# Performance work log

Measured on AMD Instinct MI355X. Metric: run time of the kernel, lower is better.

Reference implementation:

```python
import jax, jax.numpy as jnp
import numpy as np

N = 100000
E = 1600000
IN_DIM = 128
HID = 64
TDIM = 16
OUT_DIM = 2
NEG_SLOPE = 0.01  # F.leaky_relu default


def _linear_params(key, fan_in, fan_out):
    kw, kb = jax.random.split(key)
    s = 1.0 / np.sqrt(fan_in)
    w = jax.random.uniform(kw, (fan_in, fan_out), jnp.float32, -s, s)
    b = jax.random.uniform(kb, (fan_out,), jnp.float32, -s, s)
    return w, b


def setup_inputs() -> dict:
    key = jax.random.key(0)
    ks = jax.random.split(key, 12)
    x = jax.random.normal(ks[0], (N, IN_DIM), jnp.float32)
    edge_index = jax.random.randint(ks[1], (2, E), 0, N, jnp.int32)
    edge_time = jax.random.uniform(ks[2], (E, 1), jnp.float32)

    lin1_w, lin1_b = _linear_params(ks[3], IN_DIM, HID)
    attn1_w, attn1_b = _linear_params(ks[4], 2 * HID + TDIM, 1)
    t1_w, t1_b = _linear_params(ks[5], 1, TDIM)

    lin2_w, lin2_b = _linear_params(ks[6], HID, HID)
    attn2_w, attn2_b = _linear_params(ks[7], 2 * HID + TDIM, 1)
    t2_w, t2_b = _linear_params(ks[8], 1, TDIM)

    cls_w, cls_b = _linear_params(ks[9], HID, OUT_DIM)

    return dict(x=x, edge_index=edge_index, edge_time=edge_time,
                lin1_w=lin1_w, lin1_b=lin1_b, attn1_w=attn1_w, attn1_b=attn1_b,
                t1_w=t1_w, t1_b=t1_b,
                lin2_w=lin2_w, lin2_b=lin2_b, attn2_w=attn2_w, attn2_b=attn2_b,
                t2_w=t2_w, t2_b=t2_b, cls_w=cls_w, cls_b=cls_b)


def _segment_softmax(a, index, num_segments):
    # PyG softmax over variable-size neighborhoods grouped by destination node
    m = jax.ops.segment_max(a, index, num_segments=num_segments)
    e = jnp.exp(a - m[index])
    s = jax.ops.segment_sum(e, index, num_segments=num_segments)
    return e / (s[index] + 1e-16)


def _temporal_gat_conv(x, src, dst, edge_time,
                       lin_w, lin_b, attn_w, attn_b, t_w, t_b):
    # TemporalEncoding: sin(Linear(1, time_dim)(t))  -> [E, TDIM]
    t_enc = jnp.sin(edge_time @ t_w + t_b)
    # lin applied per-edge to x_i and x_j == lin applied once at node level then gathered
    h = x @ lin_w + lin_b                      # [N, HID]
    h_i = h[dst]                               # [E, HID] target features
    h_j = h[src]                               # [E, HID] source features
    alpha_in = jnp.concatenate([h_i, h_j, t_enc], axis=1)   # [E, 2*HID+TDIM]
    alpha = jax.nn.leaky_relu(alpha_in @ attn_w + attn_b, NEG_SLOPE)  # [E, 1]
    alpha = _segment_softmax(alpha, dst, x.shape[0])
    msg = h_j * alpha                          # [E, HID]
    return jax.ops.segment_sum(msg, dst, num_segments=x.shape[0])  # aggr='add'


def reference(x, edge_index, edge_time,
              lin1_w, lin1_b, attn1_w, attn1_b, t1_w, t1_b,
              lin2_w, lin2_b, attn2_w, attn2_b, t2_w, t2_b,
              cls_w, cls_b):
    src = edge_index[0]  # j (source)
    dst = edge_index[1]  # i (target / softmax segment index)
    h = _temporal_gat_conv(x, src, dst, edge_time,
                           lin1_w, lin1_b, attn1_w, attn1_b, t1_w, t1_b)
    h = jax.nn.relu(h)
    # dropout p=0.3 is identity in eval mode
    h = _temporal_gat_conv(h, src, dst, edge_time,
                           lin2_w, lin2_b, attn2_w, attn2_b, t2_w, t2_b)
    return h @ cls_w + cls_b  # [N, OUT_DIM]
```

## Files before the change

kernel.cpp:

```cpp
#include <hip/hip_runtime.h>

typedef unsigned short u16;
typedef unsigned int u32;

typedef __attribute__((ext_vector_type(8))) short short8v;
typedef __attribute__((ext_vector_type(4))) float float4v;

__device__ __forceinline__ float bf2f(u16 u) {
    return __uint_as_float(((u32)u) << 16);
}
__device__ __forceinline__ u16 f2bf(float f) {
    u32 u = __float_as_uint(f);
    u32 r = (u + 0x7fffu + ((u >> 16) & 1u)) >> 16;
    return (u16)r;
}
__device__ __forceinline__ float ldf(const void* p, int i, int isf32) {
    return isf32 ? ((const float*)p)[i] : bf2f(((const u16*)p)[i]);
}

#define P_W1   0
#define P_W2   8192
#define P_B1   12288
#define P_B2   12352
#define P_A1W  12416
#define P_A1B  12560
#define P_T1W  12561
#define P_T1B  12577
#define P_A2W  12593
#define P_A2B  12737
#define P_T2W  12738
#define P_T2B  12754
#define P_CLSW 12770
#define P_CLSB 12898
#define P_TOT  12900

#define CH   4096
#define NCHB 256
#define CAP  128

#define W1F_ELEMS 16384
#define W2F_ELEMS 8192

__global__ __launch_bounds__(256) void detect_dtype(
    const u32* __restrict__ xw, int nwords, int* __restrict__ flag)
{
    __shared__ int sbad;
    if (threadIdx.x == 0) sbad = 0;
    __syncthreads();
    int bad = 0;
    for (int i = threadIdx.x; i < nwords; i += 256) {
        u32 w = xw[i];
        int ea = (w >> 7) & 0xff;
        if (ea >= 0xF0) bad = 1;
    }
    if (bad) sbad = 1;
    __syncthreads();
    if (threadIdx.x == 0) flag[0] = sbad;
}

__global__ __launch_bounds__(256) void prep_params(
    const void* l1w, const void* l1b, const void* a1w, const void* a1b,
    const void* t1w, const void* t1b, const void* l2w, const void* l2b,
    const void* a2w, const void* a2b, const void* t2w, const void* t2b,
    const void* clsw, const void* clsb,
    const int* __restrict__ flag, float* __restrict__ P)
{
    const int f = flag[0];
    const int t = blockIdx.x * 256 + threadIdx.x;
    const int stride = gridDim.x * 256;
#define SEG(src, off, cnt) for (int i = t; i < (cnt); i += stride) P[(off) + i] = ldf(src, i, f)
    SEG(l1w, P_W1, 8192);
    SEG(l2w, P_W2, 4096);
    SEG(l1b, P_B1, 64);
    SEG(l2b, P_B2, 64);
    SEG(a1w, P_A1W, 144);
    SEG(a1b, P_A1B, 1);
    SEG(t1w, P_T1W, 16);
    SEG(t1b, P_T1B, 16);
    SEG(a2w, P_A2W, 144);
    SEG(a2b, P_A2B, 1);
    SEG(t2w, P_T2W, 16);
    SEG(t2b, P_T2B, 16);
    SEG(clsw, P_CLSW, 128);
    SEG(clsb, P_CLSB, 2);
#undef SEG
}

__global__ __launch_bounds__(256) void prep_wfrags(
    const float* __restrict__ P,
    u16* __restrict__ w1h, u16* __restrict__ w1l,
    u16* __restrict__ w2h, u16* __restrict__ w2l)
{
    int e = blockIdx.x * 256 + threadIdx.x;
    if (e >= W1F_ELEMS + W2F_ELEMS) return;
    int idx, woff;
    u16 *dh, *dl;
    if (e < W1F_ELEMS) { idx = e; woff = P_W1; dh = w1h; dl = w1l; }
    else { idx = e - W1F_ELEMS; woff = P_W2; dh = w2h; dl = w2l; }
    int j = idx & 7;
    int l = (idx >> 3) & 63;
    int ctks = idx >> 9;
    int ct = ctks & 3;
    int ks = ctks >> 2;
    int k = ks * 32 + (l >> 4) * 8 + j;
    int col = ct * 16 + (l & 15);
    float wv = P[woff + k * 64 + col];
    u16 hh = f2bf(wv);
    dh[idx] = hh;
    dl[idx] = f2bf(wv - bf2f(hh));
}

template<int K, int XMODE>
__global__ __launch_bounds__(256) void node_gemm_mfma(
    const void* __restrict__ xin, const float* __restrict__ P,
    int BOFF, int AOFF, const int* __restrict__ flag,
    const u16* __restrict__ wfh, const u16* __restrict__ wfl,
    u32* __restrict__ houtb, float* __restrict__ si, float* __restrict__ sj,
    int nnodes)
{
    const int l = threadIdx.x & 63;
    const int w = threadIdx.x >> 6;
    const int cl = l & 15;
    const int cg = l >> 4;
    const int rowbase = blockIdx.x * 64 + w * 16;
    const bool xf32 = (XMODE == 0) ? (flag[0] != 0) : false;

    const int arow = rowbase + cl;
    const int arc = (arow < nnodes) ? arow : 0;
    const int kb = cg * 8;

    const u16* xb = (const u16*)xin;
    const float* xf = (const float*)xin;
    const short8v* bhp = (const short8v*)wfh;
    const short8v* blp = (const short8v*)wfl;

    float4v acc[4];
    #pragma unroll
    for (int ct = 0; ct < 4; ++ct) acc[ct] = (float4v){0.f, 0.f, 0.f, 0.f};

    #pragma unroll
    for (int ks = 0; ks < K / 32; ++ks) {
        short8v ah, al_;
        bool hasl = false;
        if (XMODE == 2 || !xf32) {
            ah = *(const short8v*)&xb[(size_t)arc * K + ks * 32 + kb];
            al_ = (short8v){0, 0, 0, 0, 0, 0, 0, 0};
        } else {
            float4 v0 = *(const float4*)&xf[(size_t)arc * K + ks * 32 + kb];
            float4 v1 = *(const float4*)&xf[(size_t)arc * K + ks * 32 + kb + 4];
            float fv[8] = { v0.x, v0.y, v0.z, v0.w, v1.x, v1.y, v1.z, v1.w };
            #pragma unroll
            for (int j = 0; j < 8; ++j) {
                u16 hh = f2bf(fv[j]);
                ah[j] = (short)hh;
                al_[j] = (short)f2bf(fv[j] - bf2f(hh));
            }
            hasl = true;
        }
        #pragma unroll
        for (int ct = 0; ct < 4; ++ct) {
            short8v bh = bhp[(ks * 4 + ct) * 64 + l];
            short8v bl = blp[(ks * 4 + ct) * 64 + l];
            acc[ct] = __builtin_amdgcn_mfma_f32_16x16x32_bf16(ah, bh, acc[ct], 0, 0, 0);
            acc[ct] = __builtin_amdgcn_mfma_f32_16x16x32_bf16(ah, bl, acc[ct], 0, 0, 0);
            if (hasl)
                acc[ct] = __builtin_amdgcn_mfma_f32_16x16x32_bf16(al_, bh, acc[ct], 0, 0, 0);
        }
    }

    #pragma unroll
    for (int r = 0; r < 4; ++r) {
        int node = rowbase + cg * 4 + r;
        float aiv = 0.f, ajv = 0.f;
        u16 hs[4];
        #pragma unroll
        for (int ct = 0; ct < 4; ++ct) {
            float v = acc[ct][r] + P[BOFF + ct * 16 + cl];
            aiv = fmaf(v, P[AOFF + ct * 16 + cl], aiv);
            ajv = fmaf(v, P[AOFF + 64 + ct * 16 + cl], ajv);
            hs[ct] = f2bf(v);
        }
        #pragma unroll
        for (int o = 1; o < 16; o <<= 1) {
            aiv += __shfl_xor(aiv, o);
            ajv += __shfl_xor(ajv, o);
        }
        if (node < nnodes) {
            u16* hp = (u16*)houtb + (size_t)node * 64 + cl;
            hp[0] = hs[0]; hp[16] = hs[1]; hp[32] = hs[2]; hp[48] = hs[3];
            if (cl == 0) { si[node] = aiv; sj[node] = ajv; }
        }
    }
}

__global__ __launch_bounds__(256) void count_chunks(
    const int* __restrict__ eid, int* __restrict__ chunkhist, int E)
{
    __shared__ int hist[NCHB];
    const int t = threadIdx.x, c = blockIdx.x;
    hist[t] = 0;
    __syncthreads();
    const int base = c * CH;
    #pragma unroll
    for (int i = 0; i < CH / 256; ++i) {
        int e = base + t + i * 256;
        if (e < E) atomicAdd(&hist[eid[e] >> 9], 1);
    }
    __syncthreads();
    chunkhist[c * NCHB + t] = hist[t];
}

__global__ __launch_bounds__(256) void scan_chunks(
    int* __restrict__ chunkhist, int* __restrict__ buckettot, int nchunks)
{
    __shared__ int s[512];
    const int b = blockIdx.x, t = threadIdx.x;
    int v0 = (t < nchunks) ? chunkhist[(size_t)t * NCHB + b] : 0;
    int v1 = (t + 256 < nchunks) ? chunkhist[(size_t)(t + 256) * NCHB + b] : 0;
    s[t] = v0; s[t + 256] = v1;
    __syncthreads();
    for (int off = 1; off < 512; off <<= 1) {
        int x0 = (t >= off) ? s[t - off] : 0;
        int x1 = s[t + 256 - off];
        __syncthreads();
        s[t] += x0; s[t + 256] += x1;
        __syncthreads();
    }
    if (t < nchunks) chunkhist[(size_t)t * NCHB + b] = s[t] - v0;
    if (t + 256 < nchunks) chunkhist[(size_t)(t + 256) * NCHB + b] = s[t + 256] - v1;
    if (t == 255) buckettot[b] = s[511];
}

__global__ __launch_bounds__(256) void bucket_start_scan(
    const int* __restrict__ buckettot, int* __restrict__ bucketstart,
    int* __restrict__ offs, int N)
{
    __shared__ int s[NCHB];
    const int b = threadIdx.x;
    int v = buckettot[b];
    s[b] = v;
    __syncthreads();
    for (int off = 1; off < NCHB; off <<= 1) {
        int x = (b >= off) ? s[b - off] : 0;
        __syncthreads();
        s[b] += x;
        __syncthreads();
    }
    bucketstart[b] = s[b] - v;
    if (b == NCHB - 1) { bucketstart[NCHB] = s[b]; offs[N] = s[b]; }
}

__global__ __launch_bounds__(256) void place_chunks(
    const int* __restrict__ ei, const void* __restrict__ et,
    const int* __restrict__ flag, const int* __restrict__ chunkhist,
    const int* __restrict__ bucketstart, int2* __restrict__ staging, int E)
{
    __shared__ int2 sorted[CH];
    __shared__ unsigned char bno[CH];
    __shared__ int hist[NCHB], lstart[NCHB], cur[NCHB], gb[NCHB];
    const int t = threadIdx.x, c = blockIdx.x;
    const int base = c * CH;
    const int f = flag[0];
    hist[t] = 0;
    gb[t] = bucketstart[t] + chunkhist[c * NCHB + t];
    __syncthreads();
    #pragma unroll
    for (int i = 0; i < CH / 256; ++i) {
        int e = base + t + i * 256;
        if (e < E) atomicAdd(&hist[ei[E + e] >> 9], 1);
    }
    __syncthreads();
    int v = hist[t];
    lstart[t] = v;
    __syncthreads();
    for (int off = 1; off < NCHB; off <<= 1) {
        int x = (t >= off) ? lstart[t - off] : 0;
        __syncthreads();
        lstart[t] += x;
        __syncthreads();
    }
    int ex = lstart[t] - v;
    __syncthreads();
    lstart[t] = ex;
    cur[t] = ex;
    __syncthreads();
    #pragma unroll
    for (int i = 0; i < CH / 256; ++i) {
        int e = base + t + i * 256;
        if (e < E) {
            int s_ = ei[e], d = ei[E + e];
            float tt = ldf(et, e, f);
            int b = d >> 9;
            int p = atomicAdd(&cur[b], 1);
            sorted[p] = make_int2(s_ | ((d & 511) << 17), __float_as_int(tt));
            bno[p] = (unsigned char)b;
        }
    }
    __syncthreads();
    const int cnt_tot = min(CH, E - base);
    for (int idx = t; idx < cnt_tot; idx += 256) {
        int b = bno[idx];
        staging[gb[b] + (idx - lstart[b])] = sorted[idx];
    }
}

__global__ __launch_bounds__(256) void bin_edges(
    const int2* __restrict__ staging, const int* __restrict__ bucketstart,
    int* __restrict__ offs, int2* __restrict__ csrA, int N)
{
    __shared__ int cnt[512], loc[512];
    const int b = blockIdx.x, t = threadIdx.x;
    const int beg = bucketstart[b], end = bucketstart[b + 1];
    const int nstart = b << 9;
    cnt[t] = 0; cnt[t + 256] = 0;
    __syncthreads();
    for (int i = beg + t; i < end; i += 256)
        atomicAdd(&cnt[(((u32)staging[i].x) >> 17) & 511], 1);
    __syncthreads();
    int v0 = cnt[t], v1 = cnt[t + 256];
    loc[t] = v0; loc[t + 256] = v1;
    __syncthreads();
    for (int off = 1; off < 512; off <<= 1) {
        int x0 = (t >= off) ? loc[t - off] : 0;
        int x1 = loc[t + 256 - off];
        __syncthreads();
        loc[t] += x0; loc[t + 256] += x1;
        __syncthreads();
    }
    int cur0 = beg + loc[t] - v0;
    int cur1 = beg + loc[t + 256] - v1;
    if (nstart + t < N) offs[nstart + t] = cur0;
    if (nstart + t + 256 < N) offs[nstart + t + 256] = cur1;
    cnt[t] = cur0; cnt[t + 256] = cur1;
    __syncthreads();
    for (int i = beg + t; i < end; i += 256) {
        int2 e = staging[i];
        int slot = atomicAdd(&cnt[(((u32)e.x) >> 17) & 511], 1);
        csrA[slot] = make_int2(e.x & 0x1ffff, e.y);
    }
}

__global__ __launch_bounds__(256) void temporal_pass(
    int2* __restrict__ csrA, int2* __restrict__ csrB,
    const float* __restrict__ P, int E)
{
    int i = blockIdx.x * 256 + threadIdx.x;
    if (i >= E) return;
    int2 e = csrA[i];
    float tt = __int_as_float(e.y);
    float td1 = P[P_A1B], td2 = P[P_A2B];
    #pragma unroll
    for (int k = 0; k < 16; ++k) {
        td1 += __sinf(fmaf(tt, P[P_T1W + k], P[P_T1B + k])) * P[P_A1W + 128 + k];
        td2 += __sinf(fmaf(tt, P[P_T2W + k], P[P_T2B + k])) * P[P_A2W + 128 + k];
    }
    csrA[i] = make_int2(e.x, __float_as_int(td1));
    csrB[i] = make_int2(e.x, __float_as_int(td2));
}

template<int MODE>
__global__ __launch_bounds__(256) void aggregate(
    const int* __restrict__ offs, const int2* __restrict__ csr2,
    const u32* __restrict__ hb,
    const float* __restrict__ si, const float* __restrict__ sjv,
    const float* __restrict__ P,
    u32* __restrict__ houtb, void* __restrict__ outp,
    const int* __restrict__ flag, int n)
{
    __shared__ int2 cache[4][2][CAP];
    const int wave = threadIdx.x >> 6;
    const int lane = threadIdx.x & 63;
    const int half = lane >> 5;
    const int hl = lane & 31;
    const int node = blockIdx.x * 8 + wave * 2 + half;
    const bool active = node < n;
    int beg = 0, end = 0;
    if (active) { beg = offs[node]; end = offs[node + 1]; }
    const int deg = end - beg;
    int2* cw = cache[wave][half];
    const float sii = active ? si[node] : 0.f;

    float ssum = 0.f;
    for (int idx = hl; idx < deg; idx += 32) {
        int2 st = csr2[beg + idx];
        float a = sii + sjv[st.x] + __int_as_float(st.y);
        a = (a > 0.f) ? a : 0.01f * a;
        float e = __expf(fminf(a, 80.f));
        if (idx < CAP) cw[idx] = make_int2(st.x, __float_as_int(e));
        ssum += e;
    }
    #pragma unroll
    for (int o = 16; o > 0; o >>= 1) ssum += __shfl_xor(ssum, o);

    const int degc = min(deg, CAP);
    const int degpad = (degc + 3) & ~3;
    if (hl < degpad - degc) cw[degc + hl] = make_int2(0, 0);

    float ax = 0.f, ay = 0.f;
    for (int j0 = 0; j0 < degpad; j0 += 4) {
        int2 s0 = cw[j0 + 0];
        int2 s1 = cw[j0 + 1];
        int2 s2 = cw[j0 + 2];
        int2 s3 = cw[j0 + 3];
        u32 p0 = hb[s0.x * 32 + hl];
        u32 p1 = hb[s1.x * 32 + hl];
        u32 p2 = hb[s2.x * 32 + hl];
        u32 p3 = hb[s3.x * 32 + hl];
        float e0 = __int_as_float(s0.y);
        float e1 = __int_as_float(s1.y);
        float e2 = __int_as_float(s2.y);
        float e3 = __int_as_float(s3.y);
        ax = fmaf(e0, __uint_as_float(p0 << 16), ax);
        ay = fmaf(e0, __uint_as_float(p0 & 0xffff0000u), ay);
        ax = fmaf(e1, __uint_as_float(p1 << 16), ax);
        ay = fmaf(e1, __uint_as_float(p1 & 0xffff0000u), ay);
        ax = fmaf(e2, __uint_as_float(p2 << 16), ax);
        ay = fmaf(e2, __uint_as_float(p2 & 0xffff0000u), ay);
        ax = fmaf(e3, __uint_as_float(p3 << 16), ax);
        ay = fmaf(e3, __uint_as_float(p3 & 0xffff0000u), ay);
    }
    for (int j = CAP; j < deg; ++j) {
        int2 st = csr2[beg + j];
        float a = sii + sjv[st.x] + __int_as_float(st.y);
        a = (a > 0.f) ? a : 0.01f * a;
        float e = __expf(fminf(a, 80.f));
        u32 pk = hb[st.x * 32 + hl];
        ax = fmaf(e, __uint_as_float(pk << 16), ax);
        ay = fmaf(e, __uint_as_float(pk & 0xffff0000u), ay);
    }

    if (!active) return;
    float inv = 1.0f / (ssum + 1e-16f);

    if (MODE == 0) {
        float r0 = fmaxf(ax * inv, 0.f);
        float r1 = fmaxf(ay * inv, 0.f);
        houtb[node * 32 + hl] = (u32)f2bf(r0) | ((u32)f2bf(r1) << 16);
    } else {
        float r0 = ax * inv, r1 = ay * inv;
        float l0 = r0 * P[P_CLSW + 4 * hl]     + r1 * P[P_CLSW + 4 * hl + 2];
        float l1 = r0 * P[P_CLSW + 4 * hl + 1] + r1 * P[P_CLSW + 4 * hl + 3];
        #pragma unroll
        for (int o = 16; o > 0; o >>= 1) {
            l0 += __shfl_xor(l0, o);
            l1 += __shfl_xor(l1, o);
        }
        if (hl == 0) {
            l0 += P[P_CLSB];
            l1 += P[P_CLSB + 1];
            if (flag[0]) {
                ((float2*)outp)[node] = make_float2(l0, l1);
            } else {
                ((u32*)outp)[node] = (u32)f2bf(l0) | ((u32)f2bf(l1) << 16);
            }
        }
    }
}

extern "C" void kernel_launch(void* const* d_in, const int* in_sizes, int n_in,
                              void* d_out, int out_size, void* d_ws, size_t ws_size,
                              hipStream_t stream)
{
    const void* x    = d_in[0];
    const int*  ei   = (const int*)d_in[1];
    const void* et   = d_in[2];
    const void* l1w  = d_in[3];
    const void* l1b  = d_in[4];
    const void* a1w  = d_in[5];
    const void* a1b  = d_in[6];
    const void* t1w  = d_in[7];
    const void* t1b  = d_in[8];
    const void* l2w  = d_in[9];
    const void* l2b  = d_in[10];
    const void* a2w  = d_in[11];
    const void* a2b  = d_in[12];
    const void* t2w  = d_in[13];
    const void* t2b  = d_in[14];
    const void* clsw = d_in[15];
    const void* clsb = d_in[16];

    const int N = in_sizes[0] / 128;
    const int E = in_sizes[2];
    const int nchunks = (E + CH - 1) / CH;
    const int nbkt = (N + 511) >> 9;

    char* ws = (char*)d_ws;
    size_t off = 0;
    auto A = [&](size_t bytes) -> char* {
        char* p = ws + off;
        off = (off + bytes + 255) & ~(size_t)255;
        return p;
    };
    int*   flag        = (int*)A(256);
    float* P           = (float*)A(P_TOT * 4);
    u16*   w1fh        = (u16*)A(W1F_ELEMS * 2);
    u16*   w1fl        = (u16*)A(W1F_ELEMS * 2);
    u16*   w2fh        = (u16*)A(W2F_ELEMS * 2);
    u16*   w2fl        = (u16*)A(W2F_ELEMS * 2);
    u32*   h1b         = (u32*)A((size_t)N * 32 * 4);
    float* si1         = (float*)A((size_t)N * 4);
    float* sj1         = (float*)A((size_t)N * 4);
    float* si2         = (float*)A((size_t)N * 4);
    float* sj2         = (float*)A((size_t)N * 4);
    int*   chunkhist   = (int*)A((size_t)nchunks * NCHB * 4);
    int*   buckettot   = (int*)A(NCHB * 4);
    int*   bucketstart = (int*)A((size_t)(NCHB + 1) * 4);
    int*   offs        = (int*)A((size_t)(N + 1) * 4);
    int2*  csrA        = (int2*)A((size_t)E * 8);
    int2*  csrB        = (int2*)A((size_t)E * 8);
    char*  unionr      = A((size_t)E * 8 < (size_t)N * 32 * 4
                           ? (size_t)N * 32 * 4 : (size_t)E * 8);
    int2*  staging     = (int2*)unionr;
    u32*   hagb        = (u32*)unionr;
    (void)ws_size; (void)n_in; (void)out_size;

    detect_dtype<<<1, 256, 0, stream>>>((const u32*)x, 4096, flag);

    prep_params<<<32, 256, 0, stream>>>(l1w, l1b, a1w, a1b, t1w, t1b,
                                        l2w, l2b, a2w, a2b, t2w, t2b,
                                        clsw, clsb, flag, P);

    prep_wfrags<<<(W1F_ELEMS + W2F_ELEMS) / 256, 256, 0, stream>>>(
        P, w1fh, w1fl, w2fh, w2fl);

    node_gemm_mfma<128, 0><<<(N + 63) / 64, 256, 0, stream>>>(
        x, P, P_B1, P_A1W, flag, w1fh, w1fl, h1b, si1, sj1, N);

    count_chunks<<<nchunks, 256, 0, stream>>>(ei + E, chunkhist, E);

    scan_chunks<<<NCHB, 256, 0, stream>>>(chunkhist, buckettot, nchunks);

    bucket_start_scan<<<1, 256, 0, stream>>>(buckettot, bucketstart, offs, N);

    place_chunks<<<nchunks, 256, 0, stream>>>(ei, et, flag, chunkhist,
                                              bucketstart, staging, E);

    bin_edges<<<nbkt, 256, 0, stream>>>(staging, bucketstart, offs, csrA, N);

    temporal_pass<<<(E + 255) / 256, 256, 0, stream>>>(csrA, csrB, P, E);

    aggregate<0><<<(N + 7) / 8, 256, 0, stream>>>(
        offs, csrA, h1b, si1, sj1, P, hagb, nullptr, flag, N);

    node_gemm_mfma<64, 2><<<(N + 63) / 64, 256, 0, stream>>>(
        hagb, P, P_B2, P_A2W, flag, w2fh, w2fl, h1b, si2, sj2, N);

    aggregate<1><<<(N + 7) / 8, 256, 0, stream>>>(
        offs, csrB, h1b, si2, sj2, P, nullptr, d_out, flag, N);
}
```

Baseline: 299.7 us.

## Fuse temporal encoding into aggregation and merge weight-fragment prep into param prep

Removes the separate temporal_pass kernel, which read csrA and wrote both csrA and csrB over all edges. Each aggregate kernel now computes the 16-term sine time encoding inline from the raw edge time, and both layers share a single CSR buffer. prep_wfrags is folded into prep_params, so one launch is gone. The gather loop is also unrolled from 4 to 8 outstanding loads, and the fp32 high-part split now truncates instead of rounding. The inline sine work adds compute to the aggregation kernels, and the truncated high part changes which bits go into the low correction term.

```diff
diff --git a/kernel.cpp b/kernel.cpp
--- a/kernel.cpp
+++ b/kernel.cpp
@@ -63,7 +63,9 @@
     const void* t1w, const void* t1b, const void* l2w, const void* l2b,
     const void* a2w, const void* a2b, const void* t2w, const void* t2b,
     const void* clsw, const void* clsb,
-    const int* __restrict__ flag, float* __restrict__ P)
+    const int* __restrict__ flag, float* __restrict__ P,
+    u16* __restrict__ w1h, u16* __restrict__ w1l,
+    u16* __restrict__ w2h, u16* __restrict__ w2l)
 {
     const int f = flag[0];
     const int t = blockIdx.x * 256 + threadIdx.x;
@@ -84,30 +86,24 @@
     SEG(clsw, P_CLSW, 128);
     SEG(clsb, P_CLSB, 2);
 #undef SEG
-}
-
-__global__ __launch_bounds__(256) void prep_wfrags(
-    const float* __restrict__ P,
-    u16* __restrict__ w1h, u16* __restrict__ w1l,
-    u16* __restrict__ w2h, u16* __restrict__ w2l)
-{
-    int e = blockIdx.x * 256 + threadIdx.x;
-    if (e >= W1F_ELEMS + W2F_ELEMS) return;
-    int idx, woff;
-    u16 *dh, *dl;
-    if (e < W1F_ELEMS) { idx = e; woff = P_W1; dh = w1h; dl = w1l; }
-    else { idx = e - W1F_ELEMS; woff = P_W2; dh = w2h; dl = w2l; }
-    int j = idx & 7;
-    int l = (idx >> 3) & 63;
-    int ctks = idx >> 9;
-    int ct = ctks & 3;
-    int ks = ctks >> 2;
-    int k = ks * 32 + (l >> 4) * 8 + j;
-    int col = ct * 16 + (l & 15);
-    float wv = P[woff + k * 64 + col];
-    u16 hh = f2bf(wv);
-    dh[idx] = hh;
-    dl[idx] = f2bf(wv - bf2f(hh));
+    for (int e = t; e < W1F_ELEMS + W2F_ELEMS; e += stride) {
+        int idx;
+        const void* wsrc;
+        u16 *dh, *dl;
+        if (e < W1F_ELEMS) { idx = e; wsrc = l1w; dh = w1h; dl = w1l; }
+        else { idx = e - W1F_ELEMS; wsrc = l2w; dh = w2h; dl = w2l; }
+        int j = idx & 7;
+        int l = (idx >> 3) & 63;
+        int ctks = idx >> 9;
+        int ct = ctks & 3;
+        int ks = ctks >> 2;
+        int k = ks * 32 + (l >> 4) * 8 + j;
+        int col = ct * 16 + (l & 15);
+        float wv = ldf(wsrc, k * 64 + col, f);
+        u16 hh = f2bf(wv);
+        dh[idx] = hh;
+        dl[idx] = f2bf(wv - bf2f(hh));
+    }
 }
 
 template<int K, int XMODE>
@@ -151,9 +147,10 @@
             float fv[8] = { v0.x, v0.y, v0.z, v0.w, v1.x, v1.y, v1.z, v1.w };
             #pragma unroll
             for (int j = 0; j < 8; ++j) {
-                u16 hh = f2bf(fv[j]);
-                ah[j] = (short)hh;
-                al_[j] = (short)f2bf(fv[j] - bf2f(hh));
+                u32 u = __float_as_uint(fv[j]);
+                ah[j] = (short)(u >> 16);
+                float hif = __uint_as_float(u & 0xffff0000u);
+                al_[j] = (short)f2bf(fv[j] - hif);
             }
             hasl = true;
         }
@@ -340,24 +337,6 @@
     }
 }
 
-__global__ __launch_bounds__(256) void temporal_pass(
-    int2* __restrict__ csrA, int2* __restrict__ csrB,
-    const float* __restrict__ P, int E)
-{
-    int i = blockIdx.x * 256 + threadIdx.x;
-    if (i >= E) return;
-    int2 e = csrA[i];
-    float tt = __int_as_float(e.y);
-    float td1 = P[P_A1B], td2 = P[P_A2B];
-    #pragma unroll
-    for (int k = 0; k < 16; ++k) {
-        td1 += __sinf(fmaf(tt, P[P_T1W + k], P[P_T1B + k])) * P[P_A1W + 128 + k];
-        td2 += __sinf(fmaf(tt, P[P_T2W + k], P[P_T2B + k])) * P[P_A2W + 128 + k];
-    }
-    csrA[i] = make_int2(e.x, __float_as_int(td1));
-    csrB[i] = make_int2(e.x, __float_as_int(td2));
-}
-
 template<int MODE>
 __global__ __launch_bounds__(256) void aggregate(
     const int* __restrict__ offs, const int2* __restrict__ csr2,
@@ -367,6 +346,11 @@
     u32* __restrict__ houtb, void* __restrict__ outp,
     const int* __restrict__ flag, int n)
 {
+    constexpr int TW = (MODE == 0) ? P_T1W : P_T2W;
+    constexpr int TB = (MODE == 0) ? P_T1B : P_T2B;
+    constexpr int AW = (MODE == 0) ? P_A1W : P_A2W;
+    constexpr int AB = (MODE == 0) ? P_A1B : P_A2B;
+
     __shared__ int2 cache[4][2][CAP];
     const int wave = threadIdx.x >> 6;
     const int lane = threadIdx.x & 63;
@@ -383,7 +367,12 @@
     float ssum = 0.f;
     for (int idx = hl; idx < deg; idx += 32) {
         int2 st = csr2[beg + idx];
-        float a = sii + sjv[st.x] + __int_as_float(st.y);
+        float tt = __int_as_float(st.y);
+        float td = P[AB];
+        #pragma unroll
+        for (int k = 0; k < 16; ++k)
+            td += __sinf(fmaf(tt, P[TW + k], P[TB + k])) * P[AW + 128 + k];
+        float a = sii + sjv[st.x] + td;
         a = (a > 0.f) ? a : 0.01f * a;
         float e = __expf(fminf(a, 80.f));
         if (idx < CAP) cw[idx] = make_int2(st.x, __float_as_int(e));
@@ -393,35 +382,32 @@
     for (int o = 16; o > 0; o >>= 1) ssum += __shfl_xor(ssum, o);
 
     const int degc = min(deg, CAP);
-    const int degpad = (degc + 3) & ~3;
+    const int degpad = (degc + 7) & ~7;
     if (hl < degpad - degc) cw[degc + hl] = make_int2(0, 0);
 
     float ax = 0.f, ay = 0.f;
-    for (int j0 = 0; j0 < degpad; j0 += 4) {
-        int2 s0 = cw[j0 + 0];
-        int2 s1 = cw[j0 + 1];
-        int2 s2 = cw[j0 + 2];
-        int2 s3 = cw[j0 + 3];
-        u32 p0 = hb[s0.x * 32 + hl];
-        u32 p1 = hb[s1.x * 32 + hl];
-        u32 p2 = hb[s2.x * 32 + hl];
-        u32 p3 = hb[s3.x * 32 + hl];
-        float e0 = __int_as_float(s0.y);
-        float e1 = __int_as_float(s1.y);
-        float e2 = __int_as_float(s2.y);
-        float e3 = __int_as_float(s3.y);
-        ax = fmaf(e0, __uint_as_float(p0 << 16), ax);
-        ay = fmaf(e0, __uint_as_float(p0 & 0xffff0000u), ay);
-        ax = fmaf(e1, __uint_as_float(p1 << 16), ax);
-        ay = fmaf(e1, __uint_as_float(p1 & 0xffff0000u), ay);
-        ax = fmaf(e2, __uint_as_float(p2 << 16), ax);
-        ay = fmaf(e2, __uint_as_float(p2 & 0xffff0000u), ay);
-        ax = fmaf(e3, __uint_as_float(p3 << 16), ax);
-        ay = fmaf(e3, __uint_as_float(p3 & 0xffff0000u), ay);
+    for (int j0 = 0; j0 < degpad; j0 += 8) {
+        int2 sv[8];
+        u32 pv[8];
+        #pragma unroll
+        for (int q = 0; q < 8; ++q) sv[q] = cw[j0 + q];
+        #pragma unroll
+        for (int q = 0; q < 8; ++q) pv[q] = hb[sv[q].x * 32 + hl];
+        #pragma unroll
+        for (int q = 0; q < 8; ++q) {
+            float e = __int_as_float(sv[q].y);
+            ax = fmaf(e, __uint_as_float(pv[q] << 16), ax);
+            ay = fmaf(e, __uint_as_float(pv[q] & 0xffff0000u), ay);
+        }
     }
     for (int j = CAP; j < deg; ++j) {
         int2 st = csr2[beg + j];
-        float a = sii + sjv[st.x] + __int_as_float(st.y);
+        float tt = __int_as_float(st.y);
+        float td = P[AB];
+        #pragma unroll
+        for (int k = 0; k < 16; ++k)
+            td += __sinf(fmaf(tt, P[TW + k], P[TB + k])) * P[AW + 128 + k];
+        float a = sii + sjv[st.x] + td;
         a = (a > 0.f) ? a : 0.01f * a;
         float e = __expf(fminf(a, 80.f));
         u32 pk = hb[st.x * 32 + hl];
@@ -507,7 +493,6 @@
     int*   bucketstart = (int*)A((size_t)(NCHB + 1) * 4);
     int*   offs        = (int*)A((size_t)(N + 1) * 4);
     int2*  csrA        = (int2*)A((size_t)E * 8);
-    int2*  csrB        = (int2*)A((size_t)E * 8);
     char*  unionr      = A((size_t)E * 8 < (size_t)N * 32 * 4
                            ? (size_t)N * 32 * 4 : (size_t)E * 8);
     int2*  staging     = (int2*)unionr;
@@ -518,10 +503,8 @@
 
     prep_params<<<32, 256, 0, stream>>>(l1w, l1b, a1w, a1b, t1w, t1b,
                                         l2w, l2b, a2w, a2b, t2w, t2b,
-                                        clsw, clsb, flag, P);
-
-    prep_wfrags<<<(W1F_ELEMS + W2F_ELEMS) / 256, 256, 0, stream>>>(
-        P, w1fh, w1fl, w2fh, w2fl);
+                                        clsw, clsb, flag, P,
+                                        w1fh, w1fl, w2fh, w2fl);
 
     node_gemm_mfma<128, 0><<<(N + 63) / 64, 256, 0, stream>>>(
         x, P, P_B1, P_A1W, flag, w1fh, w1fl, h1b, si1, sj1, N);
@@ -537,8 +520,6 @@
 
     bin_edges<<<nbkt, 256, 0, stream>>>(staging, bucketstart, offs, csrA, N);
 
-    temporal_pass<<<(E + 255) / 256, 256, 0, stream>>>(csrA, csrB, P, E);
-
     aggregate<0><<<(N + 7) / 8, 256, 0, stream>>>(
         offs, csrA, h1b, si1, sj1, P, hagb, nullptr, flag, N);
 
@@ -546,5 +527,5 @@
         hagb, P, P_B2, P_A2W, flag, w2fh, w2fl, h1b, si2, sj2, N);
 
     aggregate<1><<<(N + 7) / 8, 256, 0, stream>>>(
-        offs, csrB, h1b, si2, sj2, P, nullptr, d_out, flag, N);
-}
+        offs, csrA, h1b, si2, sj2, P, nullptr, d_out, flag, N);
+}
```

After: 272.7 us. -9.0%, faster.
